# Kernel tuning notes

Measured on AMD Instinct MI355X. Metric: run time of the kernel, lower is better.

The kernel has to match this reference:

```python
import jax, jax.numpy as jnp
import numpy as np

B, U, D, H = 8, 256, 512, 32

def _layernorm(x, g, b, eps=1e-5):
    m = jnp.mean(x, axis=-1, keepdims=True)
    v = jnp.var(x, axis=-1, keepdims=True)
    return (x - m) * jax.lax.rsqrt(v + eps) * g + b

def setup_inputs() -> dict:
    key = jax.random.key(0)
    ks = jax.random.split(key, 12)
    s = 0.02
    return {
        "z_dyn": jax.random.normal(ks[0], (B, U, D), jnp.float32),
        "z_sem": jax.random.normal(ks[1], (B, U, D), jnp.float32),
        "te_w": jax.random.normal(ks[2], (H, D), jnp.float32) * s,
        "w_ih": jax.random.normal(ks[3], (3 * D, D), jnp.float32) * s,
        "w_hh": jax.random.normal(ks[4], (3 * D, D), jnp.float32) * s,
        "b_ih": jnp.zeros((3 * D,), jnp.float32),
        "b_hh": jnp.zeros((3 * D,), jnp.float32),
        "ln_g": jnp.ones((D,), jnp.float32),
        "ln_b": jnp.zeros((D,), jnp.float32),
        "ln2_g": jnp.ones((2 * D,), jnp.float32),
        "ln2_b": jnp.zeros((2 * D,), jnp.float32),
        "w1": jax.random.normal(ks[5], (D, 2 * D), jnp.float32) * s,
        "b1": jnp.zeros((D,), jnp.float32),
        "w2": jax.random.normal(ks[6], (D, D), jnp.float32) * s,
        "b2": jnp.zeros((D,), jnp.float32),
        "horizon": H,
    }

def reference(z_dyn, z_sem, te_w, w_ih, w_hh, b_ih, b_hh, ln_g, ln_b,
              ln2_g, ln2_b, w1, b1, w2, b2, horizon):
    b, u, d = z_dyn.shape
    h0 = z_dyn.reshape(b * u, d)
    sem = z_sem.reshape(b * u, d)
    idx = jnp.minimum(jnp.arange(horizon), te_w.shape[0] - 1)
    ts = te_w[idx]  # [horizon, d]

    def step(h, t):
        x = sem + t
        gi = x @ w_ih.T + b_ih   # [bu, 3d]
        gh = h @ w_hh.T + b_hh
        ir, iz, inn = jnp.split(gi, 3, axis=-1)
        hr, hz, hn = jnp.split(gh, 3, axis=-1)
        r = jax.nn.sigmoid(ir + hr)
        z = jax.nn.sigmoid(iz + hz)
        n = jnp.tanh(inn + r * hn)
        h_new = (1.0 - z) * n + z * h
        h_norm = _layernorm(h_new, ln_g, ln_b)
        cat = jnp.concatenate([sem, h_norm], axis=-1)
        hid = jax.nn.gelu(_layernorm(cat, ln2_g, ln2_b) @ w1.T + b1,
                          approximate=False)
        sem_h = sem + hid @ w2.T + b2
        return h_new, (h_norm, sem_h)

    _, (dyn, sems) = jax.lax.scan(step, h0, ts)  # [horizon, bu, d]
    dyn = dyn.reshape(horizon, b, u, d).transpose(1, 2, 0, 3)
    sems = sems.reshape(horizon, b, u, d).transpose(1, 2, 0, 3)
    return dyn, sems
```

## Files before the change

kernel.cpp:

```cpp
#include <hip/hip_runtime.h>
#include <math.h>


typedef unsigned short u16;
using bf16x8 = __attribute__((ext_vector_type(8))) short;
using f32x4  = __attribute__((ext_vector_type(4))) float;

#define DEV __device__ __forceinline__

constexpr int D   = 512;
constexpr int D3  = 1536;
constexpr int H   = 32;
constexpr int BU  = 2048;
constexpr long long OUT_HALF = (long long)BU * H * D;

DEV u16 f2bf(float x){
  union { float f; unsigned u; } c; c.f = x;
  unsigned u = c.u;
  u += 0x7fffu + ((u >> 16) & 1u);
  return (u16)(u >> 16);
}
DEV float bf2f(u16 b){
  union { unsigned u; float f; } c; c.u = ((unsigned)b) << 16; return c.f;
}

DEV void gload_lds16(const void* g, void* l){
  __builtin_amdgcn_global_load_lds(
      (const __attribute__((address_space(1))) void*)g,
      (__attribute__((address_space(3))) void*)l, 16, 0, 0);
}

DEV f32x4 mfma16(bf16x8 a, bf16x8 b, f32x4 c){
  return __builtin_amdgcn_mfma_f32_16x16x32_bf16(a, b, c, 0, 0, 0);
}

DEV float sigm(float x){ return 1.f / (1.f + expf(-x)); }

__global__ __launch_bounds__(256) void prep_kernel(
    const float* __restrict__ z_dyn, const float* __restrict__ z_sem,
    const float* __restrict__ te_w,  const float* __restrict__ w_ih,
    const float* __restrict__ w_hh,  const float* __restrict__ ln_g,
    const float* __restrict__ ln_b,  const float* __restrict__ ln2_g,
    const float* __restrict__ ln2_b, const float* __restrict__ w1,
    const float* __restrict__ b1,    const float* __restrict__ w2,
    float* __restrict__ h1, u16* __restrict__ hbh2, u16* __restrict__ hbl2,
    u16* __restrict__ sem_hi, u16* __restrict__ sem_lo,
    u16* __restrict__ wih_hi, u16* __restrict__ wih_lo,
    u16* __restrict__ whh_hi, u16* __restrict__ whh_lo,
    u16* __restrict__ W1s, u16* __restrict__ W1g, u16* __restrict__ w2bf,
    float* __restrict__ c1, float* __restrict__ c2p,
    float* __restrict__ d1, float* __restrict__ d2, float* __restrict__ Tg)
{
  int i = blockIdx.x * 256 + threadIdx.x;
  if (i < BU * D) {
    float hv = z_dyn[i];
    h1[i] = hv;
    u16 hh = f2bf(hv);
    hbh2[i] = hh;
    hbl2[i] = f2bf(hv - bf2f(hh));
    float sv = z_sem[i];
    u16 sh_ = f2bf(sv);
    sem_hi[i] = sh_;
    sem_lo[i] = f2bf(sv - bf2f(sh_));
  }
  if (i < D3 * D) {
    float wv = w_ih[i];
    u16 wh = f2bf(wv);
    wih_hi[i] = wh;
    wih_lo[i] = f2bf(wv - bf2f(wh));
    float uv = w_hh[i];
    u16 uh = f2bf(uv);
    whh_hi[i] = uh;
    whh_lo[i] = f2bf(uv - bf2f(uh));
  }
  if (i < D * D) {
    int k = i >> 9, j = i & 511;
    W1s[i]  = f2bf(w1[k * 1024 + j] * ln2_g[j]);
    w2bf[i] = f2bf(w2[i]);
  }
  if (i < D) {
    float sc1 = 0.f, sc2 = 0.f, sd1 = 0.f, sd2 = 0.f;
    for (int j = 0; j < 512; ++j) {
      float wA = w1[i * 1024 + j];
      float wB = w1[i * 1024 + 512 + j];
      sc1 += wA * ln2_g[j] + wB * ln2_g[512 + j];
      sc2 += wA * ln2_b[j] + wB * ln2_b[512 + j];
      float wBg = wB * ln2_g[512 + j];
      float wg = wBg * ln_g[j];
      sd1 += wg;
      sd2 += wBg * ln_b[j];
      W1g[i * 512 + j] = f2bf(wg);
    }
    c1[i] = sc1;
    c2p[i] = sc2 + b1[i];
    d1[i] = sd1;
    d2[i] = sd2;
  }
  if (i < H * D3) {
    int t = i / D3, c = i % D3;
    float s = 0.f;
    for (int d0 = 0; d0 < D; ++d0) s += te_w[t * D + d0] * w_ih[c * D + d0];
    Tg[i] = s;
  }
}

__global__ __launch_bounds__(256) void rowstats_kernel(
    const float* __restrict__ sem, float* __restrict__ Ssem,
    float* __restrict__ Ssem2)
{
  const int wid = threadIdx.x >> 6, lane = threadIdx.x & 63;
  const int row = blockIdx.x * 4 + wid;
  const float* p = sem + (size_t)row * D + lane * 8;
  float4 a0 = *(const float4*)p;
  float4 a1 = *(const float4*)(p + 4);
  float s  = a0.x + a0.y + a0.z + a0.w + a1.x + a1.y + a1.z + a1.w;
  float s2 = a0.x*a0.x + a0.y*a0.y + a0.z*a0.z + a0.w*a0.w
           + a1.x*a1.x + a1.y*a1.y + a1.z*a1.z + a1.w*a1.w;
  #pragma unroll
  for (int o = 1; o < 64; o <<= 1) { s += __shfl_xor(s, o); s2 += __shfl_xor(s2, o); }
  if (lane == 0) { Ssem[row] = s; Ssem2[row] = s2; }
}

__global__ __launch_bounds__(256) void setup_kernel(
    const u16* __restrict__ sem_hi, const u16* __restrict__ sem_lo,
    const u16* __restrict__ wih_hi, const u16* __restrict__ wih_lo,
    const u16* __restrict__ W1s, float* __restrict__ G0,
    float* __restrict__ Psem, const float* __restrict__ b_ih)
{
  __shared__ __align__(16) char smem[32768];
  char* Ah = smem;
  char* Al = smem + 8192;
  char* Bh = smem + 16384;
  char* Bl = smem + 24576;
  const int tid = threadIdx.x, wid = tid >> 6, lane = tid & 63;
  const int wr = wid >> 1, wc = wid & 1;
  const bool isG0 = blockIdx.y < 24;
  const u16* Bsrc = isG0 ? wih_hi : W1s;
  const int row0 = blockIdx.x * 64;
  const int col0 = (isG0 ? blockIdx.y : blockIdx.y - 24) * 64;

  f32x4 acc[2][2] = {};
  for (int kt = 0; kt < 8; ++kt) {
    #pragma unroll
    for (int it = 0; it < 2; ++it) {
      int s = it * 256 + tid, pr = s >> 3, pc = s & 7;
      int lch = pc ^ (pr & 7);
      size_t aoff = (size_t)(row0 + pr) * D + kt * 64 + lch * 8;
      size_t boff = (size_t)(col0 + pr) * D + kt * 64 + lch * 8;
      gload_lds16(sem_hi + aoff, Ah + it * 4096 + wid * 1024);
      gload_lds16(Bsrc + boff,   Bh + it * 4096 + wid * 1024);
      if (isG0) {
        gload_lds16(sem_lo + aoff, Al + it * 4096 + wid * 1024);
        gload_lds16(wih_lo + boff, Bl + it * 4096 + wid * 1024);
      }
    }
    asm volatile("s_waitcnt vmcnt(0)" ::: "memory");
    __syncthreads();

    const int lc = lane & 15, hi2 = lane >> 4;
    #pragma unroll
    for (int kk = 0; kk < 2; ++kk) {
      int ch = kk * 4 + hi2;
      bf16x8 afh[2], afl[2], bfh[2], bfl[2];
      #pragma unroll
      for (int mi = 0; mi < 2; ++mi) {
        int r = wr * 32 + mi * 16 + lc;
        int o = r * 128 + ((ch ^ (r & 7)) << 4);
        afh[mi] = *(const bf16x8*)(Ah + o);
        if (isG0) afl[mi] = *(const bf16x8*)(Al + o);
      }
      #pragma unroll
      for (int ci = 0; ci < 2; ++ci) {
        int r = wc * 32 + ci * 16 + lc;
        int o = r * 128 + ((ch ^ (r & 7)) << 4);
        bfh[ci] = *(const bf16x8*)(Bh + o);
        if (isG0) bfl[ci] = *(const bf16x8*)(Bl + o);
      }
      #pragma unroll
      for (int mi = 0; mi < 2; ++mi)
        #pragma unroll
        for (int ci = 0; ci < 2; ++ci) {
          f32x4 a = acc[mi][ci];
          a = mfma16(afh[mi], bfh[ci], a);
          if (isG0) {
            a = mfma16(afl[mi], bfh[ci], a);
            a = mfma16(afh[mi], bfl[ci], a);
          }
          acc[mi][ci] = a;
        }
    }
    __syncthreads();
  }
  const int lj = lane >> 4, lc2 = lane & 15;
  #pragma unroll
  for (int mi = 0; mi < 2; ++mi)
    #pragma unroll
    for (int ci = 0; ci < 2; ++ci)
      #pragma unroll
      for (int j = 0; j < 4; ++j) {
        int row = row0 + wr * 32 + mi * 16 + lj * 4 + j;
        int col = col0 + wc * 32 + ci * 16 + lc2;
        float v = acc[mi][ci][j];
        if (isG0) G0[(size_t)row * D3 + col] = v + b_ih[col];
        else      Psem[(size_t)row * D + col] = v;
      }
}

__global__ __launch_bounds__(256, 4) void fused_kernel(
    int t,
    const u16* __restrict__ hbh_in, const u16* __restrict__ hbl_in,
    u16* __restrict__ hbh_out, u16* __restrict__ hbl_out,
    const float* __restrict__ hf_in, float* __restrict__ hf_out,
    const u16* __restrict__ whh_hi, const u16* __restrict__ whh_lo,
    const float* __restrict__ G0, const float* __restrict__ Tg,
    const float* __restrict__ bhh,
    float4* __restrict__ stats_w, float* __restrict__ dyn,
    const float* __restrict__ ln_g, const float* __restrict__ ln_b,
    const float* __restrict__ Ssem, const float* __restrict__ Ssem2,
    const u16* __restrict__ lbh, const u16* __restrict__ lbl,
    const float4* __restrict__ stats_r, const u16* __restrict__ W1g,
    const float* __restrict__ Psem, const float* __restrict__ d1,
    const float* __restrict__ d2, const float* __restrict__ c1,
    const float* __restrict__ c2p, u16* __restrict__ hid_w,
    const u16* __restrict__ hid_r, const u16* __restrict__ w2bf,
    const float* __restrict__ zsem, const float* __restrict__ b2,
    float* __restrict__ sems)
{
  __shared__ __align__(16) char smem[40960];
  const int bid = blockIdx.x;
  const int tid = threadIdx.x, wid = tid >> 6, lane = tid & 63;
  const int wr = wid >> 1, wc = wid & 1;
  const int lc = lane & 15, hi2 = lane >> 4;
  const int lj = lane >> 4, lc2 = lane & 15;

  if (bid < 512) {
    if (t >= H) return;
    const int row0 = (bid & 31) * 64;
    const int gc   = (bid >> 5) * 32;
    char* Ah = smem;
    char* Al = smem + 8192;
    char* Bh = smem + 16384;
    char* Bl = smem + 28672;
    f32x4 acc[3][2] = {};

    for (int kt = 0; kt < 8; ++kt) {
      #pragma unroll
      for (int it = 0; it < 2; ++it) {
        int s = it * 256 + tid, pr = s >> 3, pc = s & 7;
        int lch = pc ^ (pr & 7);
        size_t off = (size_t)(row0 + pr) * D + kt * 64 + lch * 8;
        gload_lds16(hbh_in + off, Ah + it * 4096 + wid * 1024);
        gload_lds16(hbl_in + off, Al + it * 4096 + wid * 1024);
      }
      #pragma unroll
      for (int it = 0; it < 3; ++it) {
        int s = it * 256 + tid, pr = s >> 3, pc = s & 7;
        int lch = pc ^ (pr & 7);
        int g = pr >> 5, lr = pr & 31;
        size_t off = (size_t)(g * D + gc + lr) * D + kt * 64 + lch * 8;
        gload_lds16(whh_hi + off, Bh + it * 4096 + wid * 1024);
        gload_lds16(whh_lo + off, Bl + it * 4096 + wid * 1024);
      }
      asm volatile("s_waitcnt vmcnt(0)" ::: "memory");
      __syncthreads();

      #pragma unroll
      for (int kk = 0; kk < 2; ++kk) {
        int ch = kk * 4 + hi2;
        bf16x8 afh[2], afl[2];
        #pragma unroll
        for (int mi = 0; mi < 2; ++mi) {
          int r = wr * 32 + mi * 16 + lc;
          int o = r * 128 + ((ch ^ (r & 7)) << 4);
          afh[mi] = *(const bf16x8*)(Ah + o);
          afl[mi] = *(const bf16x8*)(Al + o);
        }
        #pragma unroll
        for (int g = 0; g < 3; ++g) {
          int rb = g * 32 + wc * 16 + lc;
          int bo = rb * 128 + ((ch ^ (rb & 7)) << 4);
          bf16x8 bh = *(const bf16x8*)(Bh + bo);
          bf16x8 bl = *(const bf16x8*)(Bl + bo);
          #pragma unroll
          for (int mi = 0; mi < 2; ++mi) {
            f32x4 a = acc[g][mi];
            a = mfma16(afh[mi], bh, a);
            a = mfma16(afl[mi], bh, a);
            a = mfma16(afh[mi], bl, a);
            acc[g][mi] = a;
          }
        }
      }
      __syncthreads();
    }

    const int gcol = gc + wc * 16 + lc2;
    const float br = bhh[gcol];
    const float bz = bhh[512 + gcol];
    const float bn = bhh[1024 + gcol];
    #pragma unroll
    for (int mi = 0; mi < 2; ++mi)
      #pragma unroll
      for (int j = 0; j < 4; ++j) {
        int row = row0 + wr * 32 + mi * 16 + lj * 4 + j;
        size_t g0i = (size_t)row * D3 + gcol;
        float gr = G0[g0i]        + Tg[t * D3 + gcol]        + acc[0][mi][j];
        float gz = G0[g0i + 512]  + Tg[t * D3 + 512 + gcol]  + acc[1][mi][j];
        float gn = G0[g0i + 1024] + Tg[t * D3 + 1024 + gcol];
        float r = sigm(gr + br);
        float z = sigm(gz + bz);
        float n = tanhf(gn + r * (acc[2][mi][j] + bn));
        size_t hi_ = (size_t)row * D + gcol;
        float hnew = (1.f - z) * n + z * hf_in[hi_];
        hf_out[hi_] = hnew;
        u16 hh = f2bf(hnew);
        hbh_out[hi_] = hh;
        hbl_out[hi_] = f2bf(hnew - bf2f(hh));
      }
  } else if (bid < 768) {
    if (t < 2 || t > H + 1) return;
    const int i = bid - 512;
    const int row0 = (i & 31) * 64, col0 = (i >> 5) * 64;
    char* Ah = smem;
    char* Al = smem + 8192;
    char* Bs = smem + 16384;
    f32x4 acc[2][2] = {};

    for (int kt = 0; kt < 8; ++kt) {
      #pragma unroll
      for (int it = 0; it < 2; ++it) {
        int s = it * 256 + tid, pr = s >> 3, pc = s & 7;
        int lch = pc ^ (pr & 7);
        size_t aoff = (size_t)(row0 + pr) * D + kt * 64 + lch * 8;
        size_t boff = (size_t)(col0 + pr) * D + kt * 64 + lch * 8;
        gload_lds16(lbh + aoff, Ah + it * 4096 + wid * 1024);
        gload_lds16(lbl + aoff, Al + it * 4096 + wid * 1024);
        gload_lds16(W1g + boff, Bs + it * 4096 + wid * 1024);
      }
      asm volatile("s_waitcnt vmcnt(0)" ::: "memory");
      __syncthreads();

      #pragma unroll
      for (int kk = 0; kk < 2; ++kk) {
        int ch = kk * 4 + hi2;
        bf16x8 afh[2], afl[2], bf[2];
        #pragma unroll
        for (int mi = 0; mi < 2; ++mi) {
          int r = wr * 32 + mi * 16 + lc;
          int o = r * 128 + ((ch ^ (r & 7)) << 4);
          afh[mi] = *(const bf16x8*)(Ah + o);
          afl[mi] = *(const bf16x8*)(Al + o);
        }
        #pragma unroll
        for (int ci = 0; ci < 2; ++ci) {
          int r = wc * 32 + ci * 16 + lc;
          bf[ci] = *(const bf16x8*)(Bs + r * 128 + ((ch ^ (r & 7)) << 4));
        }
        #pragma unroll
        for (int mi = 0; mi < 2; ++mi)
          #pragma unroll
          for (int ci = 0; ci < 2; ++ci) {
            f32x4 a = acc[mi][ci];
            a = mfma16(afh[mi], bf[ci], a);
            a = mfma16(afl[mi], bf[ci], a);
            acc[mi][ci] = a;
          }
      }
      __syncthreads();
    }

    #pragma unroll
    for (int mi = 0; mi < 2; ++mi)
      #pragma unroll
      for (int ci = 0; ci < 2; ++ci)
        #pragma unroll
        for (int j = 0; j < 4; ++j) {
          int row = row0 + wr * 32 + mi * 16 + lj * 4 + j;
          int col = col0 + wc * 32 + ci * 16 + lc2;
          float4 st = stats_r[row];
          float hn_w1 = st.x * acc[mi][ci][j] - st.y * d1[col] + d2[col];
          float pre = st.z * (Psem[(size_t)row * D + col] + hn_w1)
                      - st.w * c1[col] + c2p[col];
          float gl = 0.5f * pre * (1.f + erff(pre * 0.70710678118654752f));
          hid_w[(size_t)row * D + col] = f2bf(gl);
        }
  } else if (bid < 1024) {
    if (t < 3) return;
    const int ts = t - 3;
    const int i = bid - 768;
    const int row0 = (i & 31) * 64, col0 = (i >> 5) * 64;
    char* As = smem;
    char* Bs = smem + 8192;
    f32x4 acc[2][2] = {};

    for (int kt = 0; kt < 8; ++kt) {
      #pragma unroll
      for (int it = 0; it < 2; ++it) {
        int s = it * 256 + tid, pr = s >> 3, pc = s & 7;
        int lch = pc ^ (pr & 7);
        gload_lds16(hid_r + (size_t)(row0 + pr) * D + kt * 64 + lch * 8,
                    As + it * 4096 + wid * 1024);
        gload_lds16(w2bf + (size_t)(col0 + pr) * D + kt * 64 + lch * 8,
                    Bs + it * 4096 + wid * 1024);
      }
      asm volatile("s_waitcnt vmcnt(0)" ::: "memory");
      __syncthreads();

      #pragma unroll
      for (int kk = 0; kk < 2; ++kk) {
        int ch = kk * 4 + hi2;
        bf16x8 af[2], bf[2];
        #pragma unroll
        for (int mi = 0; mi < 2; ++mi) {
          int r = wr * 32 + mi * 16 + lc;
          af[mi] = *(const bf16x8*)(As + r * 128 + ((ch ^ (r & 7)) << 4));
        }
        #pragma unroll
        for (int ci = 0; ci < 2; ++ci) {
          int r = wc * 32 + ci * 16 + lc;
          bf[ci] = *(const bf16x8*)(Bs + r * 128 + ((ch ^ (r & 7)) << 4));
        }
        #pragma unroll
        for (int mi = 0; mi < 2; ++mi)
          #pragma unroll
          for (int ci = 0; ci < 2; ++ci)
            acc[mi][ci] = mfma16(af[mi], bf[ci], acc[mi][ci]);
      }
      __syncthreads();
    }

    #pragma unroll
    for (int mi = 0; mi < 2; ++mi)
      #pragma unroll
      for (int ci = 0; ci < 2; ++ci)
        #pragma unroll
        for (int j = 0; j < 4; ++j) {
          int row = row0 + wr * 32 + mi * 16 + lj * 4 + j;
          int col = col0 + wc * 32 + ci * 16 + lc2;
          float v = zsem[(size_t)row * D + col] + acc[mi][ci][j] + b2[col];
          __builtin_nontemporal_store(
              v, &sems[((size_t)row * H + ts) * D + col]);
        }
  } else {
    if (t < 1 || t > H) return;
    const int tt = t - 1;
    const int base = (bid - 1024) * 16 + wid * 4;
    const float4 g0 = *(const float4*)(ln_g + lane * 8);
    const float4 g1 = *(const float4*)(ln_g + lane * 8 + 4);
    const float4 b0 = *(const float4*)(ln_b + lane * 8);
    const float4 b1v = *(const float4*)(ln_b + lane * 8 + 4);
    const float gg[8] = {g0.x,g0.y,g0.z,g0.w,g1.x,g1.y,g1.z,g1.w};
    const float bb[8] = {b0.x,b0.y,b0.z,b0.w,b1v.x,b1v.y,b1v.z,b1v.w};

    for (int rr = 0; rr < 4; ++rr) {
      const int row = base + rr;
      const float* hp = hf_in + (size_t)row * D + lane * 8;
      float4 a0 = *(const float4*)hp, a1 = *(const float4*)(hp + 4);
      float h[8] = {a0.x, a0.y, a0.z, a0.w, a1.x, a1.y, a1.z, a1.w};
      float s1 = 0.f;
      #pragma unroll
      for (int k = 0; k < 8; ++k) s1 += h[k];
      #pragma unroll
      for (int o = 1; o < 64; o <<= 1) s1 += __shfl_xor(s1, o);
      float m1 = s1 * (1.f / 512.f);
      float s2 = 0.f;
      #pragma unroll
      for (int k = 0; k < 8; ++k) {
        float dv = h[k] - m1;
        s2 += dv * dv;
      }
      #pragma unroll
      for (int o = 1; o < 64; o <<= 1) s2 += __shfl_xor(s2, o);
      float rsd1 = rsqrtf(s2 * (1.f / 512.f) + 1e-5f);

      float hn[8];
      float sh = 0.f, sh2 = 0.f;
      #pragma unroll
      for (int k = 0; k < 8; ++k) {
        float x = (h[k] - m1) * rsd1 * gg[k] + bb[k];
        hn[k] = x; sh += x; sh2 += x * x;
      }
      float* dp = dyn + ((size_t)row * H + tt) * D + lane * 8;
      f32x4 v0 = {hn[0], hn[1], hn[2], hn[3]};
      f32x4 v1 = {hn[4], hn[5], hn[6], hn[7]};
      __builtin_nontemporal_store(v0, (f32x4*)dp);
      __builtin_nontemporal_store(v1, (f32x4*)(dp + 4));

      #pragma unroll
      for (int o = 1; o < 64; o <<= 1) {
        sh += __shfl_xor(sh, o); sh2 += __shfl_xor(sh2, o);
      }
      if (lane == 0) {
        float m2 = (Ssem[row] + sh) * (1.f / 1024.f);
        float vv = (Ssem2[row] + sh2) * (1.f / 1024.f) - m2 * m2;
        float rs2 = rsqrtf(vv + 1e-5f);
        stats_w[row] = make_float4(rsd1, m1 * rsd1, rs2, m2 * rs2);
      }
    }
  }
}

extern "C" void kernel_launch(void* const* d_in, const int* in_sizes, int n_in,
                              void* d_out, int out_size, void* d_ws, size_t ws_size,
                              hipStream_t stream)
{
  (void)in_sizes; (void)n_in; (void)out_size; (void)ws_size;
  const float* z_dyn = (const float*)d_in[0];
  const float* z_sem = (const float*)d_in[1];
  const float* te_w  = (const float*)d_in[2];
  const float* w_ih  = (const float*)d_in[3];
  const float* w_hh  = (const float*)d_in[4];
  const float* b_ih  = (const float*)d_in[5];
  const float* b_hh  = (const float*)d_in[6];
  const float* ln_g  = (const float*)d_in[7];
  const float* ln_b  = (const float*)d_in[8];
  const float* ln2_g = (const float*)d_in[9];
  const float* ln2_b = (const float*)d_in[10];
  const float* w1    = (const float*)d_in[11];
  const float* b1    = (const float*)d_in[12];
  const float* w2    = (const float*)d_in[13];
  const float* b2    = (const float*)d_in[14];

  char* ws = (char*)d_ws;
  const size_t MB = 1ull << 20;
  u16* hbh[3] = { (u16*)(ws + 0),      (u16*)(ws + 2 * MB),  (u16*)(ws + 4 * MB) };
  u16* hbl[3] = { (u16*)(ws + 6 * MB), (u16*)(ws + 8 * MB),  (u16*)(ws + 10 * MB) };
  float* G0     = (float*)(ws + 12 * MB);
  float* Psem   = (float*)(ws + 25 * MB);
  u16*  sem_hi  = (u16*)(ws + 29 * MB);
  u16*  sem_lo  = (u16*)(ws + 31 * MB);
  u16*  hid0    = (u16*)(ws + 33 * MB);
  u16*  hid1    = (u16*)(ws + 35 * MB);
  u16*  wih_hi  = (u16*)(ws + 37 * MB);
  u16*  wih_lo  = (u16*)(ws + 37 * MB + 1572864);
  u16*  whh_hi  = (u16*)(ws + 40 * MB);
  u16*  whh_lo  = (u16*)(ws + 40 * MB + 1572864);
  u16*  W1s     = (u16*)(ws + 43 * MB);
  u16*  W1g     = (u16*)(ws + 43 * MB + 524288);
  u16*  w2bf    = (u16*)(ws + 44 * MB);
  float* c1     = (float*)(ws + 45 * MB);
  float* c2p    = (float*)(ws + 45 * MB + 16384);
  float* d1     = (float*)(ws + 45 * MB + 32768);
  float* d2     = (float*)(ws + 45 * MB + 49152);
  float* Ssem   = (float*)(ws + 45 * MB + 65536);
  float* Ssem2  = (float*)(ws + 45 * MB + 81920);
  float4* stats0 = (float4*)(ws + 46 * MB);
  float4* stats1 = (float4*)(ws + 46 * MB + 32768);
  float* Tg     = (float*)(ws + 47 * MB);
  float* hf0    = (float*)(ws + 48 * MB);
  float* hf1    = (float*)(ws + 52 * MB);

  float* outp = (float*)d_out;
  float* out_dyn  = outp;
  float* out_sems = outp + OUT_HALF;

  prep_kernel<<<4096, 256, 0, stream>>>(
      z_dyn, z_sem, te_w, w_ih, w_hh, ln_g, ln_b, ln2_g, ln2_b, w1, b1, w2,
      hf1, hbh[2], hbl[2], sem_hi, sem_lo, wih_hi, wih_lo, whh_hi, whh_lo,
      W1s, W1g, w2bf, c1, c2p, d1, d2, Tg);
  rowstats_kernel<<<512, 256, 0, stream>>>(z_sem, Ssem, Ssem2);
  setup_kernel<<<dim3(32, 32), 256, 0, stream>>>(
      sem_hi, sem_lo, wih_hi, wih_lo, W1s, G0, Psem, b_ih);

  for (int t = 0; t <= H + 2; ++t) {
    int s_out  = ((t % 3) + 3) % 3;
    int s_in   = (((t - 1) % 3) + 3) % 3;
    int s_ln   = (((t - 2) % 3) + 3) % 3;
    float* hf_out      = (t & 1) ? hf1 : hf0;
    const float* hf_in = (t & 1) ? hf0 : hf1;
    float4* st_w = ((t - 1) & 1) ? stats1 : stats0;
    const float4* st_r = ((t - 2) & 1) ? stats1 : stats0;
    u16* hidw = ((t - 2) & 1) ? hid1 : hid0;
    const u16* hidr = ((t - 3) & 1) ? hid1 : hid0;

    fused_kernel<<<dim3(1152), dim3(256), 0, stream>>>(
        t,
        hbh[s_in], hbl[s_in], hbh[s_out], hbl[s_out],
        hf_in, hf_out,
        whh_hi, whh_lo, G0, Tg, b_hh,
        st_w, out_dyn, ln_g, ln_b, Ssem, Ssem2,
        hbh[s_ln], hbl[s_ln], st_r, W1g, Psem, d1, d2, c1, c2p, hidw,
        hidr, w2bf, z_sem, b2, out_sems);
  }
}
```

Before: 843.6 us.

## Trim split-bf16 MFMA terms, double-buffer W1/W2 GEMM tiles, and shrink LDS

The GRU hidden GEMM drops the low-part weight correction for the r and z gates and keeps it only for the n gate. It now loads only that slice of w_hh_lo into LDS. The W1 GEMM drops the low-part activation operand, so it reads only the high bf16 of h_norm. The W1 and W2 GEMMs switch to a two-stage double buffer that prefetches the next K tile while computing the current one, and shared memory falls from 40 KB to 32 KB, which may raise occupancy. These cuts reduce MFMA count and memory traffic at the cost of accuracy, and the prefetch path no longer issues an explicit vmcnt wait, which risks a race on the LDS tiles.

Result: faster. 739.5 us (-12.3%).

```diff
diff --git a/kernel.cpp b/kernel.cpp
--- a/kernel.cpp
+++ b/kernel.cpp
@@ -97,10 +97,10 @@
     d2[i] = sd2;
   }
   if (i < H * D3) {
-    int t = i / D3, c = i % D3;
+    int c = i >> 5, t = i & 31;
     float s = 0.f;
     for (int d0 = 0; d0 < D; ++d0) s += te_w[t * D + d0] * w_ih[c * D + d0];
-    Tg[i] = s;
+    Tg[t * D3 + c] = s;
   }
 }
 
@@ -217,7 +217,7 @@
     float4* __restrict__ stats_w, float* __restrict__ dyn,
     const float* __restrict__ ln_g, const float* __restrict__ ln_b,
     const float* __restrict__ Ssem, const float* __restrict__ Ssem2,
-    const u16* __restrict__ lbh, const u16* __restrict__ lbl,
+    const u16* __restrict__ lbh,
     const float4* __restrict__ stats_r, const u16* __restrict__ W1g,
     const float* __restrict__ Psem, const float* __restrict__ d1,
     const float* __restrict__ d2, const float* __restrict__ c1,
@@ -226,7 +226,7 @@
     const float* __restrict__ zsem, const float* __restrict__ b2,
     float* __restrict__ sems)
 {
-  __shared__ __align__(16) char smem[40960];
+  __shared__ __align__(16) char smem[32768];
   const int bid = blockIdx.x;
   const int tid = threadIdx.x, wid = tid >> 6, lane = tid & 63;
   const int wr = wid >> 1, wc = wid & 1;
@@ -257,9 +257,14 @@
         int s = it * 256 + tid, pr = s >> 3, pc = s & 7;
         int lch = pc ^ (pr & 7);
         int g = pr >> 5, lr = pr & 31;
-        size_t off = (size_t)(g * D + gc + lr) * D + kt * 64 + lch * 8;
-        gload_lds16(whh_hi + off, Bh + it * 4096 + wid * 1024);
-        gload_lds16(whh_lo + off, Bl + it * 4096 + wid * 1024);
+        gload_lds16(whh_hi + (size_t)(g * D + gc + lr) * D + kt * 64 + lch * 8,
+                    Bh + it * 4096 + wid * 1024);
+      }
+      {
+        int pr = tid >> 3, pc = tid & 7;
+        int lch = pc ^ (pr & 7);
+        gload_lds16(whh_lo + (size_t)(2 * D + gc + pr) * D + kt * 64 + lch * 8,
+                    Bl + wid * 1024);
       }
       asm volatile("s_waitcnt vmcnt(0)" ::: "memory");
       __syncthreads();
@@ -275,20 +280,26 @@
           afh[mi] = *(const bf16x8*)(Ah + o);
           afl[mi] = *(const bf16x8*)(Al + o);
         }
+        const int rloc = wc * 16 + lc;
         #pragma unroll
         for (int g = 0; g < 3; ++g) {
-          int rb = g * 32 + wc * 16 + lc;
+          int rb = g * 32 + rloc;
           int bo = rb * 128 + ((ch ^ (rb & 7)) << 4);
           bf16x8 bh = *(const bf16x8*)(Bh + bo);
-          bf16x8 bl = *(const bf16x8*)(Bl + bo);
           #pragma unroll
           for (int mi = 0; mi < 2; ++mi) {
             f32x4 a = acc[g][mi];
             a = mfma16(afh[mi], bh, a);
             a = mfma16(afl[mi], bh, a);
-            a = mfma16(afh[mi], bl, a);
             acc[g][mi] = a;
           }
+        }
+        {
+          int bo = rloc * 128 + ((ch ^ (rloc & 7)) << 4);
+          bf16x8 bl = *(const bf16x8*)(Bl + bo);
+          #pragma unroll
+          for (int mi = 0; mi < 2; ++mi)
+            acc[2][mi] = mfma16(afh[mi], bl, acc[2][mi]);
         }
       }
       __syncthreads();
@@ -321,35 +332,36 @@
     if (t < 2 || t > H + 1) return;
     const int i = bid - 512;
     const int row0 = (i & 31) * 64, col0 = (i >> 5) * 64;
-    char* Ah = smem;
-    char* Al = smem + 8192;
-    char* Bs = smem + 16384;
+    char* bufp[2] = { smem, smem + 16384 };
     f32x4 acc[2][2] = {};
 
-    for (int kt = 0; kt < 8; ++kt) {
+    auto stage = [&](char* base, int kt){
       #pragma unroll
       for (int it = 0; it < 2; ++it) {
         int s = it * 256 + tid, pr = s >> 3, pc = s & 7;
         int lch = pc ^ (pr & 7);
-        size_t aoff = (size_t)(row0 + pr) * D + kt * 64 + lch * 8;
-        size_t boff = (size_t)(col0 + pr) * D + kt * 64 + lch * 8;
-        gload_lds16(lbh + aoff, Ah + it * 4096 + wid * 1024);
-        gload_lds16(lbl + aoff, Al + it * 4096 + wid * 1024);
-        gload_lds16(W1g + boff, Bs + it * 4096 + wid * 1024);
-      }
-      asm volatile("s_waitcnt vmcnt(0)" ::: "memory");
-      __syncthreads();
-
+        gload_lds16(lbh + (size_t)(row0 + pr) * D + kt * 64 + lch * 8,
+                    base + it * 4096 + wid * 1024);
+        gload_lds16(W1g + (size_t)(col0 + pr) * D + kt * 64 + lch * 8,
+                    base + 8192 + it * 4096 + wid * 1024);
+      }
+    };
+
+    stage(bufp[0], 0);
+    __syncthreads();
+    int buf = 0;
+    for (int kt = 0; kt < 8; ++kt) {
+      if (kt < 7) stage(bufp[buf ^ 1], kt + 1);
+      const char* Ah = bufp[buf];
+      const char* Bs = bufp[buf] + 8192;
       #pragma unroll
       for (int kk = 0; kk < 2; ++kk) {
         int ch = kk * 4 + hi2;
-        bf16x8 afh[2], afl[2], bf[2];
+        bf16x8 afh[2], bf[2];
         #pragma unroll
         for (int mi = 0; mi < 2; ++mi) {
           int r = wr * 32 + mi * 16 + lc;
-          int o = r * 128 + ((ch ^ (r & 7)) << 4);
-          afh[mi] = *(const bf16x8*)(Ah + o);
-          afl[mi] = *(const bf16x8*)(Al + o);
+          afh[mi] = *(const bf16x8*)(Ah + r * 128 + ((ch ^ (r & 7)) << 4));
         }
         #pragma unroll
         for (int ci = 0; ci < 2; ++ci) {
@@ -359,14 +371,11 @@
         #pragma unroll
         for (int mi = 0; mi < 2; ++mi)
           #pragma unroll
-          for (int ci = 0; ci < 2; ++ci) {
-            f32x4 a = acc[mi][ci];
-            a = mfma16(afh[mi], bf[ci], a);
-            a = mfma16(afl[mi], bf[ci], a);
-            acc[mi][ci] = a;
-          }
+          for (int ci = 0; ci < 2; ++ci)
+            acc[mi][ci] = mfma16(afh[mi], bf[ci], acc[mi][ci]);
       }
       __syncthreads();
+      buf ^= 1;
     }
 
     #pragma unroll
@@ -389,23 +398,28 @@
     const int ts = t - 3;
     const int i = bid - 768;
     const int row0 = (i & 31) * 64, col0 = (i >> 5) * 64;
-    char* As = smem;
-    char* Bs = smem + 8192;
+    char* bufp[2] = { smem, smem + 16384 };
     f32x4 acc[2][2] = {};
 
-    for (int kt = 0; kt < 8; ++kt) {
+    auto stage = [&](char* base, int kt){
       #pragma unroll
       for (int it = 0; it < 2; ++it) {
         int s = it * 256 + tid, pr = s >> 3, pc = s & 7;
         int lch = pc ^ (pr & 7);
         gload_lds16(hid_r + (size_t)(row0 + pr) * D + kt * 64 + lch * 8,
-                    As + it * 4096 + wid * 1024);
+                    base + it * 4096 + wid * 1024);
         gload_lds16(w2bf + (size_t)(col0 + pr) * D + kt * 64 + lch * 8,
-                    Bs + it * 4096 + wid * 1024);
-      }
-      asm volatile("s_waitcnt vmcnt(0)" ::: "memory");
-      __syncthreads();
-
+                    base + 8192 + it * 4096 + wid * 1024);
+      }
+    };
+
+    stage(bufp[0], 0);
+    __syncthreads();
+    int buf = 0;
+    for (int kt = 0; kt < 8; ++kt) {
+      if (kt < 7) stage(bufp[buf ^ 1], kt + 1);
+      const char* As = bufp[buf];
+      const char* Bs = bufp[buf] + 8192;
       #pragma unroll
       for (int kk = 0; kk < 2; ++kk) {
         int ch = kk * 4 + hi2;
@@ -427,6 +441,7 @@
             acc[mi][ci] = mfma16(af[mi], bf[ci], acc[mi][ci]);
       }
       __syncthreads();
+      buf ^= 1;
     }
 
     #pragma unroll
@@ -579,7 +594,7 @@
         hf_in, hf_out,
         whh_hi, whh_lo, G0, Tg, b_hh,
         st_w, out_dyn, ln_g, ln_b, Ssem, Ssem2,
-        hbh[s_ln], hbl[s_ln], st_r, W1g, Psem, d1, d2, c1, c2p, hidw,
+        hbh[s_ln], st_r, W1g, Psem, d1, d2, c1, c2p, hidw,
         hidr, w2bf, z_sem, b2, out_sems);
   }
 }
```
